# Optimization experiments

Measured on AMD Instinct MI355X. Metric: run time of the kernel, lower is better.

The kernel has to match this reference:

```python
import jax, jax.numpy as jnp
import numpy as np


def setup_inputs() -> dict:
    key = jax.random.key(0)
    ks = jax.random.split(key, 8)
    N, E, H, C, L, G = 100000, 1600000, 128, 10, 5, 64
    x = jax.random.normal(ks[0], (N, H), dtype=jnp.float32)
    edge_index = jax.random.randint(ks[1], (2, E), 0, N, dtype=jnp.int32)
    batch = jnp.sort(jax.random.randint(ks[2], (N,), 0, G, dtype=jnp.int32))
    # Glorot-ish init scale for stability
    Ws = jax.random.normal(ks[3], (L, H, H), dtype=jnp.float32) * (1.0 / np.sqrt(H))
    bs = jax.random.normal(ks[4], (L, H), dtype=jnp.float32) * 0.01
    W_out = jax.random.normal(ks[5], (H, C), dtype=jnp.float32) * (1.0 / np.sqrt(H))
    b_out = jax.random.normal(ks[6], (C,), dtype=jnp.float32) * 0.01
    return {"x": x, "edge_index": edge_index, "batch": batch, "num_graphs": G,
            "Ws": Ws, "bs": bs, "W_out": W_out, "b_out": b_out}


def reference(x, edge_index, batch, num_graphs, Ws, bs, W_out, b_out):
    N = x.shape[0]
    # --- GCN normalization (add self-loops, symmetric deg^-1/2 norm), computed once ---
    loop = jnp.arange(N, dtype=edge_index.dtype)
    src = jnp.concatenate([edge_index[0], loop])  # message sources (x_j)
    dst = jnp.concatenate([edge_index[1], loop])  # aggregation targets
    deg = jax.ops.segment_sum(jnp.ones_like(dst, dtype=x.dtype), dst, num_segments=N)
    dis = jnp.where(deg > 0, jax.lax.rsqrt(jnp.maximum(deg, 1.0)), 0.0)
    norm = dis[src] * dis[dst]  # [E+N]
    # --- stacked GCNConv + ReLU ---
    for l in range(Ws.shape[0]):
        xw = x @ Ws[l]                                   # [N, H] dense transform
        msg = norm[:, None] * xw[src]                    # gather + scale per edge
        x = jax.nn.relu(jax.ops.segment_sum(msg, dst, num_segments=N) + bs[l])
    # --- global mean pool over graphs ---
    sums = jax.ops.segment_sum(x, batch, num_segments=num_graphs)       # [G, H]
    cnts = jax.ops.segment_sum(jnp.ones((N,), x.dtype), batch, num_segments=num_graphs)
    pooled = sums / jnp.maximum(cnts, 1.0)[:, None]
    return pooled @ W_out + b_out
```

## Files before the change

kernel.cpp:

```cpp
#include <hip/hip_runtime.h>
#include <hip/hip_bf16.h>
#include <stdint.h>

#define HDIM 128
#define SBITS 8
#define SBMASK 255
#define SBMAX 512

typedef __attribute__((ext_vector_type(8))) short short8;
typedef __attribute__((ext_vector_type(4))) float f32x4;
typedef __attribute__((ext_vector_type(2))) float f32x2;

__device__ __forceinline__ ushort f2bf(float f) {
  uint u = __float_as_uint(f);
  u = (u + 0x7fffu + ((u >> 16) & 1u)) >> 16;
  return (ushort)u;
}
__device__ __forceinline__ float bflo(uint v) { return __uint_as_float(v << 16); }
__device__ __forceinline__ float bfhi(uint v) { return __uint_as_float(v & 0xffff0000u); }

__device__ __forceinline__ int pdeg4(int c) { return (c + 4) & ~3; }

__device__ __forceinline__ uint pack_cw(int src, float w) {
  uint w15 = (__float_as_uint(w) + 0x8000u) >> 16;
  return (uint)src | (w15 << 17);
}
__device__ __forceinline__ uint cw_src(uint u) { return u & 0x1FFFFu; }
__device__ __forceinline__ float cw_w(uint u) { return __uint_as_float((u >> 17) << 16); }


__global__ __launch_bounds__(256) void bucket_edges(const int* __restrict__ ei,
                                                    int* __restrict__ bktcur,
                                                    uint* __restrict__ bkt, int E,
                                                    int cap) {
  __shared__ int hist[SBMAX], base[SBMAX];
  const int t = threadIdx.x;
  const int c0 = blockIdx.x * 2048;
  for (int i = t; i < SBMAX; i += 256) hist[i] = 0;
  __syncthreads();
  uint pk[8];
  int sb_[8], rk[8];
#pragma unroll
  for (int j = 0; j < 8; ++j) {
    int idx = c0 + j * 256 + t;
    sb_[j] = -1;
    if (idx < E) {
      int s = ei[idx];
      int d = ei[E + idx];
      int b = d >> SBITS;
      pk[j] = (uint)(d & SBMASK) | ((uint)s << SBITS);
      sb_[j] = b;
      rk[j] = atomicAdd(&hist[b], 1);
    }
  }
  __syncthreads();
  for (int i = t; i < SBMAX; i += 256)
    base[i] = hist[i] ? atomicAdd(&bktcur[i * 16], hist[i]) : 0;
  __syncthreads();
#pragma unroll
  for (int j = 0; j < 8; ++j)
    if (sb_[j] >= 0)
      bkt[(size_t)sb_[j] * cap + base[sb_[j]] + rk[j]] = pk[j];
}

__global__ __launch_bounds__(256) void csr_count(const uint* __restrict__ bkt,
                                                 const int* __restrict__ bktcur,
                                                 float* __restrict__ dis,
                                                 int* __restrict__ degs,
                                                 int* __restrict__ sbtot, int cap,
                                                 int N) {
  __shared__ int cnt[256];
  __shared__ int red[256];
  const int sb = blockIdx.x, t = threadIdx.x;
  const int n0 = sb << SBITS;
  const int ecnt = bktcur[sb * 16];
  const uint* eb = bkt + (size_t)sb * cap;
  cnt[t] = 0;
  __syncthreads();
  for (int i = t; i < ecnt; i += 256)
    atomicAdd(&cnt[__builtin_nontemporal_load(eb + i) & SBMASK], 1);
  __syncthreads();
  int s = 0;
  const int n = n0 + t;
  if (n < N) {
    int c = cnt[t];
    degs[n] = c;
    dis[n] = rsqrtf((float)(c + 1));
    s = pdeg4(c);
  }
  red[t] = s;
  __syncthreads();
  for (int off = 128; off; off >>= 1) {
    if (t < off) red[t] += red[t + off];
    __syncthreads();
  }
  if (t == 0) sbtot[sb] = red[0];
}

__global__ __launch_bounds__(512) void scan_sb(const int* __restrict__ sbtot,
                                               int* __restrict__ sbbase,
                                               int* __restrict__ rowptr, int SB,
                                               int N) {
  __shared__ int sh[SBMAX];
  int t = threadIdx.x;
  int v = (t < SB) ? sbtot[t] : 0;
  sh[t] = v;
  __syncthreads();
  for (int off = 1; off < SBMAX; off <<= 1) {
    int add = (t >= off) ? sh[t - off] : 0;
    __syncthreads();
    sh[t] += add;
    __syncthreads();
  }
  if (t < SB) sbbase[t] = sh[t] - v;
  if (t == SBMAX - 1) rowptr[N] = sh[SBMAX - 1];
}

__global__ __launch_bounds__(256) void csr_place(const uint* __restrict__ bkt,
                                                 const int* __restrict__ bktcur,
                                                 const int* __restrict__ sbbase,
                                                 const float* __restrict__ dis,
                                                 const int* __restrict__ degs,
                                                 int* __restrict__ rowptr,
                                                 uint* __restrict__ colw, int cap,
                                                 int N) {
  __shared__ int cur[256];
  __shared__ int sh[256];
  const int sb = blockIdx.x, t = threadIdx.x;
  const int n0 = sb << SBITS;
  const int ecnt = bktcur[sb * 16];
  const uint* eb = bkt + (size_t)sb * cap;
  const int base = sbbase[sb];
  const int n = n0 + t;
  const int deg = (n < N) ? degs[n] : 0;
  const int v = (n < N) ? pdeg4(deg) : 0;
  sh[t] = v;
  __syncthreads();
  for (int off = 1; off < 256; off <<= 1) {
    int add = (t >= off) ? sh[t - off] : 0;
    __syncthreads();
    sh[t] += add;
    __syncthreads();
  }
  const int p = sh[t] - v;
  if (n < N) {
    rowptr[n] = base + p;
    cur[t] = p + 1;
    float dn = dis[n];
    colw[base + p] = pack_cw(n, dn * dn);
    for (int q = deg + 1; q < v; ++q) colw[base + p + q] = (uint)n;
  }
  __syncthreads();
  for (int i = t; i < ecnt; i += 256) {
    uint u = __builtin_nontemporal_load(eb + i);
    int dloc = (int)(u & SBMASK);
    int s2 = (int)(u >> SBITS);
    int pos = atomicAdd(&cur[dloc], 1);
    int d = n0 + dloc;
    colw[base + pos] = pack_cw(s2, dis[s2] * dis[d]);
  }
}

__global__ __launch_bounds__(256) void swz_w(const float* __restrict__ Ws,
                                             ushort* __restrict__ Wsw, int total) {
  int idx = blockIdx.x * 256 + threadIdx.x;
  if (idx >= total) return;
  int l = idx >> 14, r = idx & 16383;
  int j = r & 7, lane = (r >> 3) & 63, kk = (r >> 9) & 3, c = r >> 11;
  int n = c * 16 + (lane & 15);
  int k = kk * 32 + (lane >> 4) * 8 + j;
  Wsw[idx] = f2bf(Ws[l * 16384 + k * HDIM + n]);
}


template <bool F32IN>
__global__ __launch_bounds__(256) void gemm_kernel(const void* __restrict__ Xin,
                                                   const ushort* __restrict__ Wsw,
                                                   ushort* __restrict__ XW, int N,
                                                   int ntiles) {
  __shared__ ushort wlds[16384];
  __shared__ ushort clds[4][16][136];
  const int t = threadIdx.x;
  {
    const int4* src = (const int4*)Wsw;
    int4* dst = (int4*)wlds;
#pragma unroll
    for (int i = 0; i < 8; ++i) dst[t + 256 * i] = src[t + 256 * i];
  }
  __syncthreads();

  const int wave = t >> 6, lane = t & 63;
  const int kq = lane >> 4, l15 = lane & 15;

  auto loadA = [&](short8* afr, int tile) {
    const int row0 = tile * 64 + wave * 16 + l15;
#pragma unroll
    for (int kk = 0; kk < 4; ++kk) afr[kk] = short8{0, 0, 0, 0, 0, 0, 0, 0};
    if (row0 < N) {
      if constexpr (F32IN) {
        const float* arow = (const float*)Xin + (size_t)row0 * HDIM;
#pragma unroll
        for (int kk = 0; kk < 4; ++kk) {
          float4 x0 = *(const float4*)(arow + kk * 32 + kq * 8);
          float4 x1 = *(const float4*)(arow + kk * 32 + kq * 8 + 4);
          short8 f;
          f[0] = (short)f2bf(x0.x); f[1] = (short)f2bf(x0.y);
          f[2] = (short)f2bf(x0.z); f[3] = (short)f2bf(x0.w);
          f[4] = (short)f2bf(x1.x); f[5] = (short)f2bf(x1.y);
          f[6] = (short)f2bf(x1.z); f[7] = (short)f2bf(x1.w);
          afr[kk] = f;
        }
      } else {
        const short8* arow = (const short8*)((const ushort*)Xin + (size_t)row0 * HDIM);
#pragma unroll
        for (int kk = 0; kk < 4; ++kk) afr[kk] = arow[kk * 4 + kq];
      }
    }
  };

  int tile = blockIdx.x;
  if (tile >= ntiles) return;
  short8 afr[4];
  loadA(afr, tile);

  for (; tile < ntiles; tile += gridDim.x) {
    const int nt = tile + gridDim.x;
    short8 afn[4];
    if (nt < ntiles) loadA(afn, nt);

    f32x4 acc[8];
#pragma unroll
    for (int c = 0; c < 8; ++c) acc[c] = f32x4{0.f, 0.f, 0.f, 0.f};
#pragma unroll
    for (int kk = 0; kk < 4; ++kk) {
#pragma unroll
      for (int c = 0; c < 8; ++c) {
        short8 bfr = *(const short8*)(wlds + (((c * 4 + kk) * 64 + lane) << 3));
        acc[c] = __builtin_amdgcn_mfma_f32_16x16x32_bf16(afr[kk], bfr, acc[c], 0, 0, 0);
      }
    }

#pragma unroll
    for (int c = 0; c < 8; ++c) {
#pragma unroll
      for (int r = 0; r < 4; ++r)
        clds[wave][kq * 4 + r][c * 16 + l15] = f2bf(acc[c][r]);
    }
    const int grow0 = tile * 64 + wave * 16;
#pragma unroll
    for (int i = 0; i < 4; ++i) {
      int pi = i * 64 + lane;
      int row = pi >> 4, piece = pi & 15;
      if (grow0 + row < N)
        *(int4*)(XW + (size_t)(grow0 + row) * HDIM + piece * 8) =
            *(const int4*)(&clds[wave][row][piece * 8]);
    }
#pragma unroll
    for (int kk = 0; kk < 4; ++kk) afr[kk] = afn[kk];
  }
}

__global__ __launch_bounds__(256, 8) void agg_kernel(const ushort* __restrict__ XW,
                                                     const uint* __restrict__ colw,
                                                     const int* __restrict__ rowptr,
                                                     const float* __restrict__ bias,
                                                     ushort* __restrict__ Y, int N) {
  const int lane = threadIdx.x & 63;
  const int node = blockIdx.x * 4 + (threadIdx.x >> 6);
  if (node >= N) return;
  const int e = lane >> 4, c = lane & 15;
  const int beg = rowptr[node];
  const int pdeg = rowptr[node + 1] - beg;
  const int last = pdeg - 1;

  uint cw[6];
#pragma unroll
  for (int k = 0; k < 6; ++k) {
    int off = 4 * k + e;
    cw[k] = __builtin_nontemporal_load(colw + beg + (off < pdeg ? off : last));
  }
  uint4 gv[6];
#pragma unroll
  for (int k = 0; k < 6; ++k)
    gv[k] = *(const uint4*)(XW + ((size_t)cw_src(cw[k]) << 7) + c * 8);

  f32x2 acc[4];
#pragma unroll
  for (int i = 0; i < 4; ++i) acc[i] = f32x2{0.f, 0.f};

#pragma unroll
  for (int k = 0; k < 6; ++k) {
    int off = 4 * k + e;
    float w = (off < pdeg) ? cw_w(cw[k]) : 0.f;
    f32x2 wv = f32x2{w, w};
    uint4 v = gv[k];
    acc[0] = __builtin_elementwise_fma(wv, f32x2{bflo(v.x), bfhi(v.x)}, acc[0]);
    acc[1] = __builtin_elementwise_fma(wv, f32x2{bflo(v.y), bfhi(v.y)}, acc[1]);
    acc[2] = __builtin_elementwise_fma(wv, f32x2{bflo(v.z), bfhi(v.z)}, acc[2]);
    acc[3] = __builtin_elementwise_fma(wv, f32x2{bflo(v.w), bfhi(v.w)}, acc[3]);
  }
  for (int off = 24 + e; off < pdeg; off += 4) {
    uint u = __builtin_nontemporal_load(colw + beg + off);
    uint4 v = *(const uint4*)(XW + ((size_t)cw_src(u) << 7) + c * 8);
    float w = cw_w(u);
    f32x2 wv = f32x2{w, w};
    acc[0] = __builtin_elementwise_fma(wv, f32x2{bflo(v.x), bfhi(v.x)}, acc[0]);
    acc[1] = __builtin_elementwise_fma(wv, f32x2{bflo(v.y), bfhi(v.y)}, acc[1]);
    acc[2] = __builtin_elementwise_fma(wv, f32x2{bflo(v.z), bfhi(v.z)}, acc[2]);
    acc[3] = __builtin_elementwise_fma(wv, f32x2{bflo(v.w), bfhi(v.w)}, acc[3]);
  }

#pragma unroll
  for (int i = 0; i < 4; ++i) {
    acc[i].x += __shfl_xor(acc[i].x, 16, 64);
    acc[i].y += __shfl_xor(acc[i].y, 16, 64);
    acc[i].x += __shfl_xor(acc[i].x, 32, 64);
    acc[i].y += __shfl_xor(acc[i].y, 32, 64);
  }
  if (e == 0) {
    float4 b0 = *(const float4*)(bias + c * 8);
    float4 b1 = *(const float4*)(bias + c * 8 + 4);
    uint4 pk;
    pk.x = (uint)f2bf(fmaxf(acc[0].x + b0.x, 0.f)) | ((uint)f2bf(fmaxf(acc[0].y + b0.y, 0.f)) << 16);
    pk.y = (uint)f2bf(fmaxf(acc[1].x + b0.z, 0.f)) | ((uint)f2bf(fmaxf(acc[1].y + b0.w, 0.f)) << 16);
    pk.z = (uint)f2bf(fmaxf(acc[2].x + b1.x, 0.f)) | ((uint)f2bf(fmaxf(acc[2].y + b1.y, 0.f)) << 16);
    pk.w = (uint)f2bf(fmaxf(acc[3].x + b1.z, 0.f)) | ((uint)f2bf(fmaxf(acc[3].y + b1.w, 0.f)) << 16);
    *(uint4*)(Y + (size_t)node * HDIM + c * 8) = pk;
  }
}


__global__ __launch_bounds__(256) void pool_partial(const ushort* __restrict__ x,
                                                    const int* __restrict__ batch,
                                                    float* __restrict__ pooled,
                                                    int* __restrict__ gcnt, int N) {
  const int g = blockIdx.x, s = blockIdx.y;
  const int t = threadIdx.x;
  __shared__ int range[2];
  __shared__ float sums[256];
  if (t < 2) {
    int target = g + t;
    int lo = 0, hi = N;
    while (lo < hi) {
      int mid = (lo + hi) >> 1;
      if (batch[mid] < target) lo = mid + 1;
      else hi = mid;
    }
    range[t] = lo;
  }
  __syncthreads();
  int beg = range[0], end = range[1];
  if (s == 0 && t == 0) gcnt[g] = end - beg;
  int col = t & 127, half = t >> 7;
  float acc = 0.f;
  for (int n = beg + s * 2 + half; n < end; n += 16) {
    acc += __uint_as_float(((uint)x[(size_t)n * HDIM + col]) << 16);
  }
  sums[t] = acc;
  __syncthreads();
  if (t < 128) atomicAdd(&pooled[g * HDIM + t], sums[t] + sums[t + 128]);
}

__global__ __launch_bounds__(256) void out_final(const float* __restrict__ pooled,
                                                 const int* __restrict__ gcnt,
                                                 const float* __restrict__ W_out,
                                                 const float* __restrict__ b_out,
                                                 float* __restrict__ out, int G, int C) {
  int i = blockIdx.x * 256 + threadIdx.x;
  if (i >= G * C) return;
  int g = i / C, c = i - g * C;
  float inv = 1.f / (float)max(gcnt[g], 1);
  const float* pg = pooled + g * HDIM;
  float o = 0.f;
  for (int h = 0; h < HDIM; ++h) o += pg[h] * W_out[h * C + c];
  out[i] = b_out[c] + o * inv;
}


extern "C" void kernel_launch(void* const* d_in, const int* in_sizes, int n_in,
                              void* d_out, int out_size, void* d_ws, size_t ws_size,
                              hipStream_t stream) {
  (void)n_in;
  (void)ws_size;
  const float* x = (const float*)d_in[0];
  const int* ei = (const int*)d_in[1];
  const int* batch = (const int*)d_in[2];
  const float* Ws = (const float*)d_in[4];
  const float* bs = (const float*)d_in[5];
  const float* W_out = (const float*)d_in[6];
  const float* b_out = (const float*)d_in[7];
  float* out = (float*)d_out;

  const int N = in_sizes[0] / HDIM;
  const int E = in_sizes[1] / 2;
  const int L = in_sizes[5] / HDIM;
  const int C = in_sizes[7];
  const int G = out_size / C;
  const int SB = (N + SBMASK) >> SBITS;
  const int cap = E / SB + 2048;

  char* p = (char*)d_ws;
  auto carve = [&](size_t bytes) {
    char* r = p;
    p += (bytes + 255) & ~(size_t)255;
    return r;
  };
  int* bktcur = (int*)carve(SBMAX * 64);
  float* dis = (float*)carve((size_t)N * 4);
  int* degs = (int*)carve((size_t)N * 4);
  int* rowptr = (int*)carve((size_t)(N + 1) * 4);
  int* sbtot = (int*)carve(SBMAX * 4);
  int* sbbase = (int*)carve(SBMAX * 4);
  uint* bkt = (uint*)carve((size_t)SB * cap * 4);
  uint* colw = (uint*)carve(((size_t)E + 4 * (size_t)N + 64) * 4);
  ushort* Wsw = (ushort*)carve((size_t)L * HDIM * HDIM * 2);
  ushort* xw = (ushort*)carve((size_t)N * HDIM * 2);
  ushort* y0 = (ushort*)carve((size_t)N * HDIM * 2);
  ushort* y1 = (ushort*)carve((size_t)N * HDIM * 2);
  float* pooled = (float*)carve((size_t)G * HDIM * 4 + (size_t)G * 4);
  int* gcnt = (int*)(pooled + (size_t)G * HDIM);

  hipMemsetAsync(bktcur, 0, SBMAX * 64, stream);
  hipMemsetAsync(pooled, 0, (size_t)G * HDIM * 4 + (size_t)G * 4, stream);

  bucket_edges<<<(E + 2047) / 2048, 256, 0, stream>>>(ei, bktcur, bkt, E, cap);
  csr_count<<<SB, 256, 0, stream>>>(bkt, bktcur, dis, degs, sbtot, cap, N);
  scan_sb<<<1, SBMAX, 0, stream>>>(sbtot, sbbase, rowptr, SB, N);
  csr_place<<<SB, 256, 0, stream>>>(bkt, bktcur, sbbase, dis, degs, rowptr, colw, cap, N);
  swz_w<<<(L * HDIM * HDIM + 255) / 256, 256, 0, stream>>>(Ws, Wsw, L * HDIM * HDIM);

  const int ntiles = (N + 63) / 64;
  const int gb = 768;
  gemm_kernel<true><<<gb, 256, 0, stream>>>(x, Wsw, xw, N, ntiles);
  agg_kernel<<<(N + 3) / 4, 256, 0, stream>>>(xw, colw, rowptr, bs, y0, N);
  ushort* xc = y0;
  ushort* xn = y1;
  for (int l = 1; l < L; ++l) {
    gemm_kernel<false><<<gb, 256, 0, stream>>>(xc, Wsw + (size_t)l * HDIM * HDIM, xw, N, ntiles);
    agg_kernel<<<(N + 3) / 4, 256, 0, stream>>>(xw, colw, rowptr, bs + (size_t)l * HDIM, xn, N);
    ushort* tmp = xc;
    xc = xn;
    xn = tmp;
  }
  pool_partial<<<dim3(G, 8), 256, 0, stream>>>(xc, batch, pooled, gcnt, N);
  out_final<<<(G * C + 255) / 256, 256, 0, stream>>>(pooled, gcnt, W_out, b_out, out, G, C);
}
```

Before: 569.9 us.

## Keep GEMM weights in registers and specialize aggregation by padded degree

The GEMM kernel stops staging the bf16 weight matrix in LDS and instead loads each wave's weight fragments straight into registers (32 short8 per lane). Occupancy is set to 2 blocks per CU and the grid shrinks to 512 blocks. The aggregation kernel now dispatches on the padded degree to templated bulk paths with exact unroll counts (4, 5, 6 plus a tail), so only low-degree nodes keep clamping. Its launch bound drops from 8 to 3 blocks, which frees registers for deeper gathers but lowers latency hiding for this memory-bound gather.

```diff
diff --git a/kernel.cpp b/kernel.cpp
--- a/kernel.cpp
+++ b/kernel.cpp
@@ -174,23 +174,21 @@
 
 
 template <bool F32IN>
-__global__ __launch_bounds__(256) void gemm_kernel(const void* __restrict__ Xin,
-                                                   const ushort* __restrict__ Wsw,
-                                                   ushort* __restrict__ XW, int N,
-                                                   int ntiles) {
-  __shared__ ushort wlds[16384];
+__global__ __launch_bounds__(256, 2) void gemm_kernel(const void* __restrict__ Xin,
+                                                      const ushort* __restrict__ Wsw,
+                                                      ushort* __restrict__ XW, int N,
+                                                      int ntiles) {
   __shared__ ushort clds[4][16][136];
   const int t = threadIdx.x;
-  {
-    const int4* src = (const int4*)Wsw;
-    int4* dst = (int4*)wlds;
-#pragma unroll
-    for (int i = 0; i < 8; ++i) dst[t + 256 * i] = src[t + 256 * i];
-  }
-  __syncthreads();
-
   const int wave = t >> 6, lane = t & 63;
   const int kq = lane >> 4, l15 = lane & 15;
+
+  short8 bfr[4][8];
+#pragma unroll
+  for (int kk = 0; kk < 4; ++kk)
+#pragma unroll
+    for (int c = 0; c < 8; ++c)
+      bfr[kk][c] = *(const short8*)(Wsw + (((c * 4 + kk) * 64 + lane) << 3));
 
   auto loadA = [&](short8* afr, int tile) {
     const int row0 = tile * 64 + wave * 16 + l15;
@@ -234,10 +232,8 @@
 #pragma unroll
     for (int kk = 0; kk < 4; ++kk) {
 #pragma unroll
-      for (int c = 0; c < 8; ++c) {
-        short8 bfr = *(const short8*)(wlds + (((c * 4 + kk) * 64 + lane) << 3));
-        acc[c] = __builtin_amdgcn_mfma_f32_16x16x32_bf16(afr[kk], bfr, acc[c], 0, 0, 0);
-      }
+      for (int c = 0; c < 8; ++c)
+        acc[c] = __builtin_amdgcn_mfma_f32_16x16x32_bf16(afr[kk], bfr[kk][c], acc[c], 0, 0, 0);
     }
 
 #pragma unroll
@@ -260,7 +256,42 @@
   }
 }
 
-__global__ __launch_bounds__(256, 8) void agg_kernel(const ushort* __restrict__ XW,
+
+template <int K, bool CLAMP>
+__device__ __forceinline__ void agg_bulk(const ushort* __restrict__ XW,
+                                         const uint* __restrict__ colw, int beg,
+                                         int pdeg, int e, int c, f32x2* acc) {
+  const int last = pdeg - 1;
+  uint cw[K];
+#pragma unroll
+  for (int k = 0; k < K; ++k) {
+    int off = 4 * k + e;
+    if (CLAMP) off = off < pdeg ? off : last;
+    cw[k] = __builtin_nontemporal_load(colw + beg + off);
+  }
+  uint4 gv[K];
+#pragma unroll
+  for (int k = 0; k < K; ++k)
+    gv[k] = *(const uint4*)(XW + ((size_t)cw_src(cw[k]) << 7) + c * 8);
+#pragma unroll
+  for (int k = 0; k < K; ++k) {
+    float w;
+    if (CLAMP) {
+      int off = 4 * k + e;
+      w = (off < pdeg) ? cw_w(cw[k]) : 0.f;
+    } else {
+      w = cw_w(cw[k]);
+    }
+    f32x2 wv = f32x2{w, w};
+    uint4 v = gv[k];
+    acc[0] = __builtin_elementwise_fma(wv, f32x2{bflo(v.x), bfhi(v.x)}, acc[0]);
+    acc[1] = __builtin_elementwise_fma(wv, f32x2{bflo(v.y), bfhi(v.y)}, acc[1]);
+    acc[2] = __builtin_elementwise_fma(wv, f32x2{bflo(v.z), bfhi(v.z)}, acc[2]);
+    acc[3] = __builtin_elementwise_fma(wv, f32x2{bflo(v.w), bfhi(v.w)}, acc[3]);
+  }
+}
+
+__global__ __launch_bounds__(256, 3) void agg_kernel(const ushort* __restrict__ XW,
                                                      const uint* __restrict__ colw,
                                                      const int* __restrict__ rowptr,
                                                      const float* __restrict__ bias,
@@ -271,43 +302,30 @@
   const int e = lane >> 4, c = lane & 15;
   const int beg = rowptr[node];
   const int pdeg = rowptr[node + 1] - beg;
-  const int last = pdeg - 1;
-
-  uint cw[6];
-#pragma unroll
-  for (int k = 0; k < 6; ++k) {
-    int off = 4 * k + e;
-    cw[k] = __builtin_nontemporal_load(colw + beg + (off < pdeg ? off : last));
-  }
-  uint4 gv[6];
-#pragma unroll
-  for (int k = 0; k < 6; ++k)
-    gv[k] = *(const uint4*)(XW + ((size_t)cw_src(cw[k]) << 7) + c * 8);
+  const int nb = pdeg >> 2;
 
   f32x2 acc[4];
 #pragma unroll
   for (int i = 0; i < 4; ++i) acc[i] = f32x2{0.f, 0.f};
 
-#pragma unroll
-  for (int k = 0; k < 6; ++k) {
-    int off = 4 * k + e;
-    float w = (off < pdeg) ? cw_w(cw[k]) : 0.f;
-    f32x2 wv = f32x2{w, w};
-    uint4 v = gv[k];
-    acc[0] = __builtin_elementwise_fma(wv, f32x2{bflo(v.x), bfhi(v.x)}, acc[0]);
-    acc[1] = __builtin_elementwise_fma(wv, f32x2{bflo(v.y), bfhi(v.y)}, acc[1]);
-    acc[2] = __builtin_elementwise_fma(wv, f32x2{bflo(v.z), bfhi(v.z)}, acc[2]);
-    acc[3] = __builtin_elementwise_fma(wv, f32x2{bflo(v.w), bfhi(v.w)}, acc[3]);
-  }
-  for (int off = 24 + e; off < pdeg; off += 4) {
-    uint u = __builtin_nontemporal_load(colw + beg + off);
-    uint4 v = *(const uint4*)(XW + ((size_t)cw_src(u) << 7) + c * 8);
-    float w = cw_w(u);
-    f32x2 wv = f32x2{w, w};
-    acc[0] = __builtin_elementwise_fma(wv, f32x2{bflo(v.x), bfhi(v.x)}, acc[0]);
-    acc[1] = __builtin_elementwise_fma(wv, f32x2{bflo(v.y), bfhi(v.y)}, acc[1]);
-    acc[2] = __builtin_elementwise_fma(wv, f32x2{bflo(v.z), bfhi(v.z)}, acc[2]);
-    acc[3] = __builtin_elementwise_fma(wv, f32x2{bflo(v.w), bfhi(v.w)}, acc[3]);
+  if (nb == 4) {
+    agg_bulk<4, false>(XW, colw, beg, pdeg, e, c, acc);
+  } else if (nb == 5) {
+    agg_bulk<5, false>(XW, colw, beg, pdeg, e, c, acc);
+  } else if (nb >= 6) {
+    agg_bulk<6, false>(XW, colw, beg, pdeg, e, c, acc);
+    for (int off = 24 + e; off < pdeg; off += 4) {
+      uint u = __builtin_nontemporal_load(colw + beg + off);
+      uint4 v = *(const uint4*)(XW + ((size_t)cw_src(u) << 7) + c * 8);
+      float w = cw_w(u);
+      f32x2 wv = f32x2{w, w};
+      acc[0] = __builtin_elementwise_fma(wv, f32x2{bflo(v.x), bfhi(v.x)}, acc[0]);
+      acc[1] = __builtin_elementwise_fma(wv, f32x2{bflo(v.y), bfhi(v.y)}, acc[1]);
+      acc[2] = __builtin_elementwise_fma(wv, f32x2{bflo(v.z), bfhi(v.z)}, acc[2]);
+      acc[3] = __builtin_elementwise_fma(wv, f32x2{bflo(v.w), bfhi(v.w)}, acc[3]);
+    }
+  } else {
+    agg_bulk<4, true>(XW, colw, beg, pdeg, e, c, acc);
   }
 
 #pragma unroll
@@ -430,7 +448,7 @@
   swz_w<<<(L * HDIM * HDIM + 255) / 256, 256, 0, stream>>>(Ws, Wsw, L * HDIM * HDIM);
 
   const int ntiles = (N + 63) / 64;
-  const int gb = 768;
+  const int gb = 512;
   gemm_kernel<true><<<gb, 256, 0, stream>>>(x, Wsw, xw, N, ntiles);
   agg_kernel<<<(N + 3) / 4, 256, 0, stream>>>(xw, colw, rowptr, bs, y0, N);
   ushort* xc = y0;
```

After: 553.1 us. 1.03x faster.
